# Optimization experiments

Measured on AMD Instinct MI355X. Metric: run time of the kernel, lower is better.

The kernel has to match this reference:

```python
import jax, jax.numpy as jnp
import numpy as np

N_EMBD = 1024
N_FF = 4 * N_EMBD
N_EXPERTS = 8
TOP_K = 2
B, S = 1, 2048


def setup_inputs() -> dict:
    key = jax.random.key(0)
    ks = jax.random.split(key, 8)
    std = 0.02
    x = jax.random.normal(ks[0], (B, S, N_EMBD), dtype=jnp.float32)
    Wr = jax.random.normal(ks[1], (N_EMBD, N_EXPERTS), dtype=jnp.float32) * std
    br = jnp.zeros((N_EXPERTS,), dtype=jnp.float32)
    W1 = jax.random.normal(ks[2], (N_EXPERTS, N_EMBD, N_FF), dtype=jnp.float32) * std
    b1 = jnp.zeros((N_EXPERTS, N_FF), dtype=jnp.float32)
    W2 = jax.random.normal(ks[3], (N_EXPERTS, N_FF, N_EMBD), dtype=jnp.float32) * std
    b2 = jnp.zeros((N_EXPERTS, N_EMBD), dtype=jnp.float32)
    return {"x": x, "Wr": Wr, "br": br, "W1": W1, "b1": b1, "W2": W2, "b2": b2}


def reference(x, Wr, br, W1, b1, W2, b2):
    # x: [B, S, D]
    Bx, Sx, D = x.shape
    T = Bx * Sx
    E = Wr.shape[1]
    flat = x.reshape(T, D)

    # Router: softmax over experts, top-k, renormalize top-k weights
    logits = flat @ Wr + br                      # [T, E]
    probs = jax.nn.softmax(logits, axis=-1)
    topk_w, topk_i = jax.lax.top_k(probs, TOP_K)  # [T, K]
    topk_w = topk_w / jnp.sum(topk_w, axis=-1, keepdims=True)

    # Per-token combined expert weights (0 for non-selected experts).
    # Equivalent to the original gather/index_add combine.
    tok = jnp.arange(T)[:, None]
    w = jnp.zeros((T, E), dtype=flat.dtype).at[tok, topk_i].add(topk_w)  # [T, E]

    # Dense grouped expert MLP (exact GELU, matching torch nn.GELU default).
    h = jnp.einsum('td,edh->teh', flat, W1) + b1          # [T, E, 4D]
    h = jax.nn.gelu(h, approximate=False)
    y = jnp.einsum('teh,ehd->ted', h, W2) + b2            # [T, E, D]

    out = jnp.einsum('ted,te->td', y, w)                  # weighted combine
    return out.reshape(Bx, Sx, D)
```

## Files before the change

### kernel.cpp

```cpp
#include <hip/hip_runtime.h>
#include <stdint.h>

#define T_TOK 2048
#define DIM   1024
#define HID   4096
#define NEXP  8

typedef __attribute__((ext_vector_type(8))) short  short8;
typedef __attribute__((ext_vector_type(4))) short  short4v;
typedef __attribute__((ext_vector_type(4))) float  floatx4;
typedef __attribute__((ext_vector_type(4))) int    intx4;

__device__ __forceinline__ ushort f2bf(float f) {
    union { float f; uint32_t i; } v; v.f = f;
    uint32_t r = v.i + 0x7FFFu + ((v.i >> 16) & 1u);
    return (ushort)(r >> 16);
}
__device__ __forceinline__ float gelu_exact(float x) {
    return 0.5f * x * (1.0f + erff(x * 0.70710678118654752f));
}

__global__ __launch_bounds__(256) void cast_x_kernel(
    const float* __restrict__ x, ushort* __restrict__ Xb)
{
    int i = (blockIdx.x * 256 + threadIdx.x) * 8;
    floatx4 a = *(const floatx4*)(x + i);
    floatx4 b = *(const floatx4*)(x + i + 4);
    uint32_t o[4];
    o[0] = (uint32_t)f2bf(a[0]) | ((uint32_t)f2bf(a[1]) << 16);
    o[1] = (uint32_t)f2bf(a[2]) | ((uint32_t)f2bf(a[3]) << 16);
    o[2] = (uint32_t)f2bf(b[0]) | ((uint32_t)f2bf(b[1]) << 16);
    o[3] = (uint32_t)f2bf(b[2]) | ((uint32_t)f2bf(b[3]) << 16);
    *(intx4*)(Xb + i) = *(const intx4*)o;
}

__global__ __launch_bounds__(256) void router_kernel(
    const float* __restrict__ x, const float* __restrict__ Wr,
    const float* __restrict__ br, int* __restrict__ counts,
    int* __restrict__ tlist, float* __restrict__ wlist)
{
    int wv = threadIdx.x >> 6, l = threadIdx.x & 63;
    int t = blockIdx.x * 4 + wv;
    float acc[NEXP];
#pragma unroll
    for (int e = 0; e < NEXP; e++) acc[e] = 0.f;
    const float* xr = x + (size_t)t * DIM;
    for (int d = l; d < DIM; d += 64) {
        float xv = xr[d];
        floatx4 w0 = *(const floatx4*)(Wr + (size_t)d * NEXP);
        floatx4 w1 = *(const floatx4*)(Wr + (size_t)d * NEXP + 4);
#pragma unroll
        for (int e = 0; e < 4; e++) { acc[e] += xv * w0[e]; acc[e + 4] += xv * w1[e]; }
    }
#pragma unroll
    for (int e = 0; e < NEXP; e++) {
#pragma unroll
        for (int off = 32; off; off >>= 1) acc[e] += __shfl_xor(acc[e], off, 64);
    }
    if (l == 0) {
        float lg[NEXP];
#pragma unroll
        for (int e = 0; e < NEXP; e++) lg[e] = acc[e] + br[e];
        int e0 = 0;
#pragma unroll
        for (int e = 1; e < NEXP; e++) if (lg[e] > lg[e0]) e0 = e;
        int e1 = -1;
#pragma unroll
        for (int e = 0; e < NEXP; e++) {
            if (e == e0) continue;
            if (e1 < 0 || lg[e] > lg[e1]) e1 = e;
        }
        float w0 = 1.f / (1.f + expf(lg[e1] - lg[e0]));
        float w1 = 1.f - w0;
        int s0 = atomicAdd(&counts[e0], 1);
        tlist[e0 * T_TOK + s0] = t;
        wlist[e0 * T_TOK + s0] = w0;
        int s1 = atomicAdd(&counts[e1], 1);
        tlist[e1 * T_TOK + s1] = t | (1 << 16);
        wlist[e1 * T_TOK + s1] = w1;
    }
}

template <int MODE>
__global__ __launch_bounds__(256, 2) void moe_gemm(
    const ushort* __restrict__ A, const float* __restrict__ W,
    const float* __restrict__ bias, const int* __restrict__ counts,
    const int* __restrict__ tlist, const float* __restrict__ wlist,
    ushort* __restrict__ Hout, float* __restrict__ Yacc)
{
    constexpr int NTOT = MODE ? DIM : HID;
    constexpr int AROW = MODE ? HID : DIM;
    constexpr int KLEN = MODE ? 2048 : 1024;

    int bx = blockIdx.x;
    int e, mt, nt, kc;
    if (MODE == 0) { e = bx >> 9; mt = (bx >> 5) & 15; nt = bx & 31; kc = 0; }
    else { e = bx >> 8; int r = bx & 255; mt = r >> 4; nt = (r >> 1) & 7; kc = r & 1; }

    int Ne = counts[e];
    if (mt * 128 >= Ne) return;

    size_t wbase = (size_t)e * DIM * HID + (size_t)kc * 2048 * NTOT + (size_t)nt * 128;

    __shared__ ushort ldsA[128 * 40];
    __shared__ ushort ldsB[128 * 36];

    int tid = threadIdx.x;
    int wv = tid >> 6, l = tid & 63;

    const ushort* arowp[2]; int apos[2];
#pragma unroll
    for (int i = 0; i < 2; i++) {
        int idx = i * 256 + tid;
        int r = idx >> 2, p = idx & 3;
        int slot = mt * 128 + r; if (slot >= Ne) slot = Ne - 1;
        int packed = tlist[e * T_TOK + slot];
        int tok = packed & 0xFFFF, rk = (packed >> 16) & 1;
        size_t arow = MODE ? (size_t)(tok * 2 + rk) : (size_t)tok;
        arowp[i] = A + arow * AROW + (MODE ? kc * 2048 : 0) + p * 8;
        apos[i] = r * 40 + p * 8;
    }

    int kp = tid & 15;
    int n8 = tid >> 4;
    size_t boffg = wbase + (size_t)(2 * kp) * NTOT + n8 * 8;

    int wm = wv >> 1, wn = wv & 1;
    int q = l >> 4;
    int aoff[4], boff[4];
#pragma unroll
    for (int mi = 0; mi < 4; mi++)
        aoff[mi] = (wm * 64 + mi * 16 + (l & 15)) * 40 + q * 8;
#pragma unroll
    for (int ni = 0; ni < 4; ni++)
        boff[ni] = (wn * 64 + ni * 16 + (l & 15)) * 36 + q * 8;

    floatx4 zz = {0.f, 0.f, 0.f, 0.f};
    floatx4 acc[4][4];
#pragma unroll
    for (int mi = 0; mi < 4; mi++)
#pragma unroll
        for (int ni = 0; ni < 4; ni++) acc[mi][ni] = zz;

    for (int k0 = 0; k0 < KLEN; k0 += 32) {
        intx4 av[2];
#pragma unroll
        for (int i = 0; i < 2; i++) av[i] = *(const intx4*)(arowp[i] + k0);
        const float* p0 = W + boffg + (size_t)k0 * NTOT;
        const float* p1 = p0 + NTOT;
        floatx4 a0 = *(const floatx4*)(p0);
        floatx4 a1 = *(const floatx4*)(p0 + 4);
        floatx4 b0 = *(const floatx4*)(p1);
        floatx4 b1 = *(const floatx4*)(p1 + 4);
        uint32_t pr[8];
#pragma unroll
        for (int j = 0; j < 8; j++) {
            float va = (j < 4) ? a0[j & 3] : a1[j & 3];
            float vb = (j < 4) ? b0[j & 3] : b1[j & 3];
            pr[j] = (uint32_t)f2bf(va) | ((uint32_t)f2bf(vb) << 16);
        }

        __syncthreads();
#pragma unroll
        for (int i = 0; i < 2; i++) *(intx4*)&ldsA[apos[i]] = av[i];
#pragma unroll
        for (int j = 0; j < 8; j++)
            *(uint32_t*)&ldsB[(n8 * 8 + j) * 36 + 2 * kp] = pr[j];
        __syncthreads();

        short8 af[4], bf[4];
#pragma unroll
        for (int mi = 0; mi < 4; mi++) af[mi] = *(const short8*)&ldsA[aoff[mi]];
#pragma unroll
        for (int ni = 0; ni < 4; ni++) {
            short4v blo = *(const short4v*)&ldsB[boff[ni]];
            short4v bhi = *(const short4v*)&ldsB[boff[ni] + 4];
            bf[ni] = __builtin_shufflevector(blo, bhi, 0, 1, 2, 3, 4, 5, 6, 7);
        }
#pragma unroll
        for (int mi = 0; mi < 4; mi++)
#pragma unroll
            for (int ni = 0; ni < 4; ni++)
                acc[mi][ni] = __builtin_amdgcn_mfma_f32_16x16x32_bf16(
                    af[mi], bf[ni], acc[mi][ni], 0, 0, 0);
    }

#pragma unroll
    for (int mi = 0; mi < 4; mi++) {
        int rbase = wm * 64 + mi * 16 + q * 4;
#pragma unroll
        for (int j = 0; j < 4; j++) {
            int slot = mt * 128 + rbase + j;
            if (slot >= Ne) continue;
            int packed = tlist[e * T_TOK + slot];
            int tok = packed & 0xFFFF, rk = (packed >> 16) & 1;
#pragma unroll
            for (int ni = 0; ni < 4; ni++) {
                int col = nt * 128 + wn * 64 + ni * 16 + (l & 15);
                float v = acc[mi][ni][j];
                float bc = bias[e * NTOT + col];
                if (MODE == 0) {
                    v = gelu_exact(v + bc);
                    Hout[(size_t)(tok * 2 + rk) * HID + col] = f2bf(v);
                } else {
                    if (kc == 0) v += bc;
                    v *= wlist[e * T_TOK + slot];
                    atomicAdd(&Yacc[(size_t)tok * DIM + col], v);
                }
            }
        }
    }
}

__global__ __launch_bounds__(256) void combine_kernel(
    const float* __restrict__ Y, float* __restrict__ out)
{
    int i = (blockIdx.x * 256 + threadIdx.x) * 4;
    *(floatx4*)(out + i) = *(const floatx4*)(Y + i);
}

extern "C" void kernel_launch(void* const* d_in, const int* in_sizes, int n_in,
                              void* d_out, int out_size, void* d_ws, size_t ws_size,
                              hipStream_t stream) {
    const float* x  = (const float*)d_in[0];
    const float* Wr = (const float*)d_in[1];
    const float* br = (const float*)d_in[2];
    const float* W1 = (const float*)d_in[3];
    const float* b1 = (const float*)d_in[4];
    const float* W2 = (const float*)d_in[5];
    const float* b2 = (const float*)d_in[6];
    float* out = (float*)d_out;

    char* ws = (char*)d_ws;
    int*    counts = (int*)ws;
    int*    tlist  = (int*)(ws + 256);
    float*  wlist  = (float*)(ws + 256 + 65536);
    ushort* Hbuf   = (ushort*)(ws + 256 + 131072);
    float*  Yacc   = (float*)(ws + 256 + 131072 + 33554432);
    ushort* Xb     = (ushort*)Yacc;

    hipMemsetAsync(counts, 0, 256, stream);
    cast_x_kernel<<<T_TOK * DIM / 2048, 256, 0, stream>>>(x, Xb);
    router_kernel<<<T_TOK / 4, 256, 0, stream>>>(x, Wr, br, counts, tlist, wlist);
    moe_gemm<0><<<NEXP * 16 * 32, 256, 0, stream>>>(Xb, W1, b1, counts, tlist, wlist, Hbuf, nullptr);
    hipMemsetAsync(Yacc, 0, (size_t)T_TOK * DIM * sizeof(float), stream);
    moe_gemm<1><<<NEXP * 16 * 8 * 2, 256, 0, stream>>>(Hbuf, W2, b2, counts, tlist, wlist, nullptr, Yacc);
    combine_kernel<<<out_size / 1024, 256, 0, stream>>>(Yacc, out);
}
```

Baseline: 617.2 us.

## Pre-transpose and cast expert weights to bf16, load tiles via global_load_lds

Adds a kernel that transposes and casts W1/W2 into a bf16 K-major workspace buffer before each expert GEMM. A new GEMM variant then streams A and B tiles straight into LDS with global_load_lds and feeds 16x16x32 bf16 MFMAs, with atomic accumulation written directly into the output. This removes the in-GEMM fp32 weight conversion and strided loads, and drops the separate combine copy. In exchange it does an extra full pass over the fp32 weights on every call and needs a larger workspace, falling back to the old path when the workspace is too small.

```diff
diff --git a/kernel.cpp b/kernel.cpp
--- a/kernel.cpp
+++ b/kernel.cpp
@@ -18,6 +18,11 @@
 }
 __device__ __forceinline__ float gelu_exact(float x) {
     return 0.5f * x * (1.0f + erff(x * 0.70710678118654752f));
+}
+__device__ __forceinline__ void glds16(const ushort* g, ushort* lds) {
+    __builtin_amdgcn_global_load_lds(
+        (const __attribute__((address_space(1))) unsigned int*)g,
+        (__attribute__((address_space(3))) unsigned int*)lds, 16, 0, 0);
 }
 
 __global__ __launch_bounds__(256) void cast_x_kernel(
@@ -32,6 +37,34 @@
     o[2] = (uint32_t)f2bf(b[0]) | ((uint32_t)f2bf(b[1]) << 16);
     o[3] = (uint32_t)f2bf(b[2]) | ((uint32_t)f2bf(b[3]) << 16);
     *(intx4*)(Xb + i) = *(const intx4*)o;
+}
+
+__global__ __launch_bounds__(256) void transpose_cast_kernel(
+    const float* __restrict__ in, ushort* __restrict__ out, int R, int C)
+{
+    __shared__ float tile[64][65];
+    int e = blockIdx.z;
+    int rb = blockIdx.y * 64, cb = blockIdx.x * 64;
+    const float* ip = in + (size_t)e * R * C;
+    ushort* op = out + (size_t)e * R * C;
+    int t = threadIdx.x;
+    int tr = t >> 4, tc4 = (t & 15) * 4;
+#pragma unroll
+    for (int i = 0; i < 4; i++) {
+        int r = i * 16 + tr;
+        floatx4 v = *(const floatx4*)(ip + (size_t)(rb + r) * C + cb + tc4);
+        tile[r][tc4] = v[0]; tile[r][tc4 + 1] = v[1];
+        tile[r][tc4 + 2] = v[2]; tile[r][tc4 + 3] = v[3];
+    }
+    __syncthreads();
+    int cc = t >> 2, rseg = (t & 3) * 16;
+#pragma unroll
+    for (int s = 0; s < 2; s++) {
+        ushort o[8];
+#pragma unroll
+        for (int j = 0; j < 8; j++) o[j] = f2bf(tile[rseg + s * 8 + j][cc]);
+        *(intx4*)(op + (size_t)(cb + cc) * R + rb + rseg + s * 8) = *(const intx4*)o;
+    }
 }
 
 __global__ __launch_bounds__(256) void router_kernel(
@@ -78,6 +111,107 @@
         int s1 = atomicAdd(&counts[e1], 1);
         tlist[e1 * T_TOK + s1] = t | (1 << 16);
         wlist[e1 * T_TOK + s1] = w1;
+    }
+}
+
+template <int MODE>
+__global__ __launch_bounds__(256, 2) void moe_gemm2(
+    const ushort* __restrict__ A, const ushort* __restrict__ Wt,
+    const float* __restrict__ bias, const int* __restrict__ counts,
+    const int* __restrict__ tlist, const float* __restrict__ wlist,
+    ushort* __restrict__ Hout, float* __restrict__ Yout)
+{
+    constexpr int NTOT  = MODE ? DIM : HID;
+    constexpr int KFULL = MODE ? HID : DIM;
+    constexpr int KLEN  = MODE ? 2048 : 1024;
+
+    int bx = blockIdx.x;
+    int e, mt, nt, kc;
+    if (MODE == 0) { e = bx >> 9; mt = (bx >> 5) & 15; nt = bx & 31; kc = 0; }
+    else { e = bx >> 8; int rr = bx & 255; mt = rr >> 4; nt = (rr >> 1) & 7; kc = rr & 1; }
+
+    int Ne = counts[e];
+    if (mt * 128 >= Ne) return;
+
+    __shared__ ushort ldsA[4096];
+    __shared__ ushort ldsB[4096];
+
+    int tid = threadIdx.x, wv = tid >> 6, l = tid & 63;
+    int srow = (wv & 1) * 64 + l;
+    int kq = (wv >> 1) * 8;
+
+    int slot = mt * 128 + srow; if (slot >= Ne) slot = Ne - 1;
+    int packed = tlist[e * T_TOK + slot];
+    int tok = packed & 0xFFFF, rk = (packed >> 16) & 1;
+    size_t arow = MODE ? (size_t)(tok * 2 + rk) : (size_t)tok;
+    const ushort* aptr = A + arow * KFULL + kc * 2048 + kq;
+    const ushort* bptr = Wt + (size_t)e * NTOT * KFULL
+                            + (size_t)(nt * 128 + srow) * KFULL + kc * 2048 + kq;
+
+    ushort* la0 = &ldsA[wv * 512];
+    ushort* la1 = &ldsA[2048 + wv * 512];
+    ushort* lb0 = &ldsB[wv * 512];
+    ushort* lb1 = &ldsB[2048 + wv * 512];
+
+    int wm = wv >> 1, wn = wv & 1, q = l >> 4, lr = l & 15;
+    int aoff[4], boff[4];
+#pragma unroll
+    for (int mi = 0; mi < 4; mi++) aoff[mi] = q * 1024 + (wm * 64 + mi * 16 + lr) * 8;
+#pragma unroll
+    for (int ni = 0; ni < 4; ni++) boff[ni] = q * 1024 + (wn * 64 + ni * 16 + lr) * 8;
+
+    floatx4 zz = {0.f, 0.f, 0.f, 0.f};
+    floatx4 acc[4][4];
+#pragma unroll
+    for (int mi = 0; mi < 4; mi++)
+#pragma unroll
+        for (int ni = 0; ni < 4; ni++) acc[mi][ni] = zz;
+
+    for (int k0 = 0; k0 < KLEN; k0 += 32) {
+        __syncthreads();
+        glds16(aptr + k0,      la0);
+        glds16(aptr + k0 + 16, la1);
+        glds16(bptr + k0,      lb0);
+        glds16(bptr + k0 + 16, lb1);
+        __syncthreads();
+
+        short8 af[4], bfv[4];
+#pragma unroll
+        for (int mi = 0; mi < 4; mi++) af[mi] = *(const short8*)&ldsA[aoff[mi]];
+#pragma unroll
+        for (int ni = 0; ni < 4; ni++) bfv[ni] = *(const short8*)&ldsB[boff[ni]];
+#pragma unroll
+        for (int mi = 0; mi < 4; mi++)
+#pragma unroll
+            for (int ni = 0; ni < 4; ni++)
+                acc[mi][ni] = __builtin_amdgcn_mfma_f32_16x16x32_bf16(
+                    af[mi], bfv[ni], acc[mi][ni], 0, 0, 0);
+    }
+
+#pragma unroll
+    for (int mi = 0; mi < 4; mi++) {
+        int rbase = wm * 64 + mi * 16 + q * 4;
+#pragma unroll
+        for (int j = 0; j < 4; j++) {
+            int slot2 = mt * 128 + rbase + j;
+            if (slot2 >= Ne) continue;
+            int pk2 = tlist[e * T_TOK + slot2];
+            int tok2 = pk2 & 0xFFFF, rk2 = (pk2 >> 16) & 1;
+#pragma unroll
+            for (int ni = 0; ni < 4; ni++) {
+                int col = nt * 128 + wn * 64 + ni * 16 + lr;
+                float v = acc[mi][ni][j];
+                float bc = bias[e * NTOT + col];
+                if (MODE == 0) {
+                    v = gelu_exact(v + bc);
+                    Hout[(size_t)(tok2 * 2 + rk2) * HID + col] = f2bf(v);
+                } else {
+                    if (kc == 0) v += bc;
+                    v *= wlist[e * T_TOK + slot2];
+                    atomicAdd(&Yout[(size_t)tok2 * DIM + col], v);
+                }
+            }
+        }
     }
 }
 
@@ -230,20 +364,42 @@
     const float* W2 = (const float*)d_in[5];
     const float* b2 = (const float*)d_in[6];
     float* out = (float*)d_out;
-
     char* ws = (char*)d_ws;
-    int*    counts = (int*)ws;
-    int*    tlist  = (int*)(ws + 256);
-    float*  wlist  = (float*)(ws + 256 + 65536);
-    ushort* Hbuf   = (ushort*)(ws + 256 + 131072);
-    float*  Yacc   = (float*)(ws + 256 + 131072 + 33554432);
-    ushort* Xb     = (ushort*)Yacc;
-
-    hipMemsetAsync(counts, 0, 256, stream);
-    cast_x_kernel<<<T_TOK * DIM / 2048, 256, 0, stream>>>(x, Xb);
-    router_kernel<<<T_TOK / 4, 256, 0, stream>>>(x, Wr, br, counts, tlist, wlist);
-    moe_gemm<0><<<NEXP * 16 * 32, 256, 0, stream>>>(Xb, W1, b1, counts, tlist, wlist, Hbuf, nullptr);
-    hipMemsetAsync(Yacc, 0, (size_t)T_TOK * DIM * sizeof(float), stream);
-    moe_gemm<1><<<NEXP * 16 * 8 * 2, 256, 0, stream>>>(Hbuf, W2, b2, counts, tlist, wlist, nullptr, Yacc);
-    combine_kernel<<<out_size / 1024, 256, 0, stream>>>(Yacc, out);
-}
+
+    if (ws_size >= 104988928ULL) {
+        int*    counts = (int*)ws;
+        int*    tlist  = (int*)(ws + 256);
+        float*  wlist  = (float*)(ws + 65792);
+        ushort* Xb     = (ushort*)(ws + 131328);
+        ushort* Hbuf   = (ushort*)(ws + 4325632);
+        ushort* Wt     = (ushort*)(ws + 37880064);
+
+        hipMemsetAsync(counts, 0, 256, stream);
+        hipMemsetAsync(out, 0, (size_t)T_TOK * DIM * sizeof(float), stream);
+        cast_x_kernel<<<T_TOK * DIM / 2048, 256, 0, stream>>>(x, Xb);
+        router_kernel<<<T_TOK / 4, 256, 0, stream>>>(x, Wr, br, counts, tlist, wlist);
+        transpose_cast_kernel<<<dim3(HID / 64, DIM / 64, NEXP), 256, 0, stream>>>(
+            W1, Wt, DIM, HID);
+        moe_gemm2<0><<<NEXP * 16 * 32, 256, 0, stream>>>(
+            Xb, Wt, b1, counts, tlist, wlist, Hbuf, nullptr);
+        transpose_cast_kernel<<<dim3(DIM / 64, HID / 64, NEXP), 256, 0, stream>>>(
+            W2, Wt, HID, DIM);
+        moe_gemm2<1><<<NEXP * 16 * 8 * 2, 256, 0, stream>>>(
+            Hbuf, Wt, b2, counts, tlist, wlist, nullptr, out);
+    } else {
+        int*    counts = (int*)ws;
+        int*    tlist  = (int*)(ws + 256);
+        float*  wlist  = (float*)(ws + 256 + 65536);
+        ushort* Hbuf   = (ushort*)(ws + 256 + 131072);
+        float*  Yacc   = (float*)(ws + 256 + 131072 + 33554432);
+        ushort* Xb     = (ushort*)Yacc;
+
+        hipMemsetAsync(counts, 0, 256, stream);
+        cast_x_kernel<<<T_TOK * DIM / 2048, 256, 0, stream>>>(x, Xb);
+        router_kernel<<<T_TOK / 4, 256, 0, stream>>>(x, Wr, br, counts, tlist, wlist);
+        moe_gemm<0><<<NEXP * 16 * 32, 256, 0, stream>>>(Xb, W1, b1, counts, tlist, wlist, Hbuf, nullptr);
+        hipMemsetAsync(Yacc, 0, (size_t)T_TOK * DIM * sizeof(float), stream);
+        moe_gemm<1><<<NEXP * 16 * 8 * 2, 256, 0, stream>>>(Hbuf, W2, b2, counts, tlist, wlist, nullptr, Yacc);
+        combine_kernel<<<out_size / 1024, 256, 0, stream>>>(Yacc, out);
+    }
+}
```

Measured after the change: 656.9 us. 6.4% more time.
